# Kernel tuning notes

Hardware: AMD Instinct MI355X
Metric: run time of the kernel (lower is better)

The kernel has to match this reference:

```python
import jax, jax.numpy as jnp
import numpy as np
from jax import lax

B, K, C = 8, 65536, 128
NUM_PROPOSAL = 1024


def furthest_point_sample(xyz, n):
    """xyz: (B,K,3) -> (B,n) int32 indices, matching pointnet2 FPS."""
    b, k, _ = xyz.shape
    init_far = jnp.zeros((b,), dtype=jnp.int32)          # first picked point = index 0
    init_dist = jnp.full((b, k), 1e10, dtype=xyz.dtype)  # running min squared distance

    def step(carry, _):
        dist, far = carry
        pt = jnp.take_along_axis(xyz, far[:, None, None].astype(jnp.int32), axis=1)  # (B,1,3)
        d = jnp.sum((xyz - pt) ** 2, axis=-1)            # (B,K)
        dist = jnp.minimum(dist, d)
        far = jnp.argmax(dist, axis=-1).astype(jnp.int32)
        return (dist, far), far

    (_, _), rest = lax.scan(step, (init_dist, init_far), None, length=n - 1)  # rest: (n-1,B)
    inds = jnp.concatenate([init_far[None, :], rest], axis=0)                  # (n,B)
    return jnp.transpose(inds, (1, 0))                                         # (B,n)


def setup_inputs() -> dict:
    key = jax.random.key(0)
    k1, k2 = jax.random.split(key)
    xyz = jax.random.normal(k1, (B, K, 3), dtype=jnp.float32)
    features = jax.random.normal(k2, (B, C, K), dtype=jnp.float32)
    return {"xyz": xyz, "features": features}


def reference(xyz, features):
    sample_inds = furthest_point_sample(xyz, NUM_PROPOSAL)            # (B,n)
    # gather_operation(xyz^T, inds)^T -> (B,n,3)
    new_xyz = jnp.take_along_axis(xyz, sample_inds[:, :, None], axis=1)
    # gather_operation(features, inds) -> (B,C,n)
    new_features = jnp.take_along_axis(features, sample_inds[:, None, :], axis=2)
    return (new_xyz, new_features, sample_inds)
```

## Files before the change

### kernel.cpp

```cpp
#include <hip/hip_runtime.h>
#include <stdint.h>

#define BATCH 8
#define K 65536
#define CFEAT 128
#define NPROP 1024
#define M 16
#define T 256
#define PTS (K / M)
#define PPT (PTS / T)

#define OUT_FEAT (BATCH * NPROP * 3)
#define OUT_INDS (BATCH * NPROP * 3 + BATCH * CFEAT * NPROP)

#define SLOT_STRIDE 8
#define WS_ULLS (2 * BATCH * M * SLOT_STRIDE)

__global__ __launch_bounds__(256) void fps_init(unsigned long long* ws) {
    int i = blockIdx.x * 256 + threadIdx.x;
    if (i < WS_ULLS) ws[i] = 0ull;
}

__device__ __forceinline__ unsigned int wave_umax63(unsigned int x) {
    int v = (int)x;
    int t;
    t = __builtin_amdgcn_update_dpp(v, v, 0x111, 0xF, 0xF, false);
    v = ((unsigned)t > (unsigned)v) ? t : v;
    t = __builtin_amdgcn_update_dpp(v, v, 0x112, 0xF, 0xF, false);
    v = ((unsigned)t > (unsigned)v) ? t : v;
    t = __builtin_amdgcn_update_dpp(v, v, 0x114, 0xF, 0xF, false);
    v = ((unsigned)t > (unsigned)v) ? t : v;
    t = __builtin_amdgcn_update_dpp(v, v, 0x118, 0xF, 0xF, false);
    v = ((unsigned)t > (unsigned)v) ? t : v;
    t = __builtin_amdgcn_update_dpp(v, v, 0x142, 0xF, 0xF, false);
    v = ((unsigned)t > (unsigned)v) ? t : v;
    t = __builtin_amdgcn_update_dpp(v, v, 0x143, 0xF, 0xF, false);
    v = ((unsigned)t > (unsigned)v) ? t : v;
    return (unsigned int)v;
}

__device__ __forceinline__ unsigned int row16_umax15(unsigned int x) {
    int v = (int)x;
    int t;
    t = __builtin_amdgcn_update_dpp(v, v, 0x111, 0xF, 0xF, false);
    v = ((unsigned)t > (unsigned)v) ? t : v;
    t = __builtin_amdgcn_update_dpp(v, v, 0x112, 0xF, 0xF, false);
    v = ((unsigned)t > (unsigned)v) ? t : v;
    t = __builtin_amdgcn_update_dpp(v, v, 0x114, 0xF, 0xF, false);
    v = ((unsigned)t > (unsigned)v) ? t : v;
    t = __builtin_amdgcn_update_dpp(v, v, 0x118, 0xF, 0xF, false);
    v = ((unsigned)t > (unsigned)v) ? t : v;
    return (unsigned int)v;
}

__global__ __launch_bounds__(T) void fps_kernel(const float* __restrict__ xyz,
                                                float* __restrict__ out,
                                                unsigned long long* __restrict__ ws) {
    const int b = blockIdx.x & 7;
    const int w = blockIdx.x >> 3;
    const int tid = threadIdx.x;
    const int lane = tid & 63;
    const int wv = tid >> 6;
    const float* xb = xyz + (size_t)b * (K * 3);
    const int base = w * PTS;

    __shared__ unsigned long long s_wkey[T / 64];
    __shared__ int s_g;

    float px[PPT], py[PPT], pz[PPT], dist[PPT];
#pragma unroll
    for (int j = 0; j < PPT; ++j) {
        int l = j * T + tid;
        int g = base + l;
        px[j] = xb[3 * g];
        py[j] = xb[3 * g + 1];
        pz[j] = xb[3 * g + 2];
        dist[j] = 1e10f;
    }
    float qx = xb[0], qy = xb[1], qz = xb[2];
    if (w == 0 && tid == 0) out[OUT_INDS + b * NPROP] = 0.0f;

    for (int t = 1; t < NPROP; ++t) {
        float bestd = -1.0f;
        unsigned int bestl = 0;
#pragma unroll
        for (int j = 0; j < PPT; ++j) {
            float dx = __fsub_rn(px[j], qx);
            float dy = __fsub_rn(py[j], qy);
            float dz = __fsub_rn(pz[j], qz);
            float d = __fadd_rn(__fadd_rn(__fmul_rn(dx, dx), __fmul_rn(dy, dy)),
                                __fmul_rn(dz, dz));
            float nd = fminf(dist[j], d);
            dist[j] = nd;
            unsigned int l = (unsigned int)(j * T + tid);
            bool gt = nd > bestd;
            bestd = gt ? nd : bestd;
            bestl = gt ? l : bestl;
        }
        unsigned int du = __float_as_uint(bestd);
        unsigned int m1 = wave_umax63(du);
        unsigned int maxd = (unsigned int)__builtin_amdgcn_readlane((int)m1, 63);
        unsigned int cand = (du == maxd) ? ~bestl : 0u;
        unsigned int m2 = wave_umax63(cand);

        const int par = t & 1;
        unsigned long long* sgrp = ws + (size_t)((par * BATCH + b) * M) * SLOT_STRIDE;
        const unsigned int tt = (unsigned int)t;

        if (lane == 63) {
            unsigned int l = ~m2;
            unsigned int g = (unsigned int)base + l;
            s_wkey[wv] = ((unsigned long long)maxd << 32) |
                         ((unsigned long long)((0xFFFFu - g) & 0xFFFFu) << 16) |
                         (unsigned long long)tt;
        }
        __syncthreads();

        if (tid == 0) {
            unsigned long long kb = s_wkey[0];
#pragma unroll
            for (int i = 1; i < T / 64; ++i) kb = (s_wkey[i] > kb) ? s_wkey[i] : kb;
            __hip_atomic_store(&sgrp[(size_t)w * SLOT_STRIDE], kb,
                               __ATOMIC_RELAXED, __HIP_MEMORY_SCOPE_AGENT);
        }

        if (tid < M) {
            unsigned long long* sp = sgrp + (size_t)tid * SLOT_STRIDE;
            unsigned long long k;
            do {
                k = __hip_atomic_load(sp, __ATOMIC_RELAXED, __HIP_MEMORY_SCOPE_AGENT);
            } while ((unsigned short)k != (unsigned short)tt);
            unsigned int hi = (unsigned int)(k >> 32);
            unsigned int lo = (unsigned int)k;
            unsigned int p1 = row16_umax15(hi);
            unsigned int maxk = (unsigned int)__builtin_amdgcn_readlane((int)p1, 15);
            unsigned int c2 = (hi == maxk) ? lo : 0u;
            unsigned int p2 = row16_umax15(c2);
            unsigned int low = (unsigned int)__builtin_amdgcn_readlane((int)p2, 15);
            unsigned int g = 0xFFFFu - (low >> 16);
            if (tid == 0) {
                s_g = (int)g;
                if (w == 0) out[OUT_INDS + b * NPROP + t] = (float)g;
            }
        }
        __syncthreads();
        int g = s_g;
        qx = xb[3 * g];
        qy = xb[3 * g + 1];
        qz = xb[3 * g + 2];
    }
}

__global__ __launch_bounds__(256) void gather_kernel(const float* __restrict__ xyz,
                                                     const float* __restrict__ feat,
                                                     float* __restrict__ out) {
    int gid = blockIdx.x * 256 + threadIdx.x;
    int n = gid & (NPROP - 1);
    int b = gid >> 17;
    int c = (gid >> 10) & (CFEAT - 1);
    int ind = (int)out[OUT_INDS + (b << 10) + n];
    out[OUT_FEAT + gid] = feat[(((size_t)b * CFEAT + c) << 16) + (size_t)ind];
    if (gid < BATCH * NPROP) {
        int b2 = gid >> 10;
        int ind2 = (int)out[OUT_INDS + gid];
        const float* s = xyz + ((size_t)b2 * K + (size_t)ind2) * 3;
        float a0 = s[0], a1 = s[1], a2 = s[2];
        out[gid * 3 + 0] = a0;
        out[gid * 3 + 1] = a1;
        out[gid * 3 + 2] = a2;
    }
}

extern "C" void kernel_launch(void* const* d_in, const int* in_sizes, int n_in,
                              void* d_out, int out_size, void* d_ws, size_t ws_size,
                              hipStream_t stream) {
    const float* xyz = (const float*)d_in[0];
    const float* feat = (const float*)d_in[1];
    float* out = (float*)d_out;
    unsigned long long* ws = (unsigned long long*)d_ws;

    hipLaunchKernelGGL(fps_init, dim3(WS_ULLS / 256), dim3(256), 0, stream, ws);
    hipLaunchKernelGGL(fps_kernel, dim3(BATCH * M), dim3(T), 0, stream,
                       xyz, out, ws);
    hipLaunchKernelGGL(gather_kernel, dim3(BATCH * CFEAT * NPROP / 256), dim3(256),
                       0, stream, xyz, feat, out);
}
```

Measured before the change: 1.972 ms.

## Prefetch candidate coordinates during cross-block poll and use LDS atomic max

Each of the 16 polling lanes loads its own candidate's coordinates as soon as its slot is ready, then the winning lane's coordinates are broadcast with ds_bpermute. This takes the dependent global load of the winning point off the critical path after the final barrier. The per-wave key reduction now uses an LDS atomicMax instead of a serial loop in thread 0, and polling is double-issued with a wave-wide __all exit. In exchange, all 16 lanes issue extra global loads, polling traffic goes up, and the ping-pong s_kmax must be reset correctly.

```diff
diff --git a/kernel.cpp b/kernel.cpp
--- a/kernel.cpp
+++ b/kernel.cpp
@@ -60,12 +60,11 @@
     const int w = blockIdx.x >> 3;
     const int tid = threadIdx.x;
     const int lane = tid & 63;
-    const int wv = tid >> 6;
     const float* xb = xyz + (size_t)b * (K * 3);
     const int base = w * PTS;
 
-    __shared__ unsigned long long s_wkey[T / 64];
-    __shared__ int s_g;
+    __shared__ unsigned long long s_kmax[2];
+    __shared__ float s_qx, s_qy, s_qz;
 
     float px[PPT], py[PPT], pz[PPT], dist[PPT];
 #pragma unroll
@@ -78,7 +77,9 @@
         dist[j] = 1e10f;
     }
     float qx = xb[0], qy = xb[1], qz = xb[2];
+    if (tid == 0) { s_kmax[0] = 0ull; s_kmax[1] = 0ull; }
     if (w == 0 && tid == 0) out[OUT_INDS + b * NPROP] = 0.0f;
+    __syncthreads();
 
     for (int t = 1; t < NPROP; ++t) {
         float bestd = -1.0f;
@@ -110,26 +111,39 @@
         if (lane == 63) {
             unsigned int l = ~m2;
             unsigned int g = (unsigned int)base + l;
-            s_wkey[wv] = ((unsigned long long)maxd << 32) |
-                         ((unsigned long long)((0xFFFFu - g) & 0xFFFFu) << 16) |
-                         (unsigned long long)tt;
+            unsigned long long key = ((unsigned long long)maxd << 32) |
+                                     ((unsigned long long)((0xFFFFu - g) & 0xFFFFu) << 16) |
+                                     (unsigned long long)tt;
+            atomicMax(&s_kmax[par], key);
         }
         __syncthreads();
 
         if (tid == 0) {
-            unsigned long long kb = s_wkey[0];
-#pragma unroll
-            for (int i = 1; i < T / 64; ++i) kb = (s_wkey[i] > kb) ? s_wkey[i] : kb;
+            unsigned long long kb = s_kmax[par];
+            s_kmax[par] = 0ull;
             __hip_atomic_store(&sgrp[(size_t)w * SLOT_STRIDE], kb,
                                __ATOMIC_RELAXED, __HIP_MEMORY_SCOPE_AGENT);
         }
 
         if (tid < M) {
             unsigned long long* sp = sgrp + (size_t)tid * SLOT_STRIDE;
-            unsigned long long k;
-            do {
-                k = __hip_atomic_load(sp, __ATOMIC_RELAXED, __HIP_MEMORY_SCOPE_AGENT);
-            } while ((unsigned short)k != (unsigned short)tt);
+            unsigned long long a = __hip_atomic_load(sp, __ATOMIC_RELAXED,
+                                                     __HIP_MEMORY_SCOPE_AGENT);
+            unsigned long long bq = __hip_atomic_load(sp, __ATOMIC_RELAXED,
+                                                      __HIP_MEMORY_SCOPE_AGENT);
+            unsigned long long k = 0ull;
+            bool got = false;
+            for (;;) {
+                if (!got && (unsigned short)a == (unsigned short)tt) { k = a; got = true; }
+                if (__all(got)) break;
+                a = __hip_atomic_load(sp, __ATOMIC_RELAXED, __HIP_MEMORY_SCOPE_AGENT);
+                if (!got && (unsigned short)bq == (unsigned short)tt) { k = bq; got = true; }
+                if (__all(got)) break;
+                bq = __hip_atomic_load(sp, __ATOMIC_RELAXED, __HIP_MEMORY_SCOPE_AGENT);
+            }
+            unsigned int gl = 0xFFFFu - (unsigned int)((k >> 16) & 0xFFFFu);
+            const float* cp = xb + 3 * (size_t)gl;
+            float cxl = cp[0], cyl = cp[1], czl = cp[2];
             unsigned int hi = (unsigned int)(k >> 32);
             unsigned int lo = (unsigned int)k;
             unsigned int p1 = row16_umax15(hi);
@@ -138,16 +152,21 @@
             unsigned int p2 = row16_umax15(c2);
             unsigned int low = (unsigned int)__builtin_amdgcn_readlane((int)p2, 15);
             unsigned int g = 0xFFFFu - (low >> 16);
+            int s = (int)(g >> 12);
+            int ad = s << 2;
+            float wx = __uint_as_float((unsigned int)__builtin_amdgcn_ds_bpermute(
+                ad, (int)__float_as_uint(cxl)));
+            float wy = __uint_as_float((unsigned int)__builtin_amdgcn_ds_bpermute(
+                ad, (int)__float_as_uint(cyl)));
+            float wz = __uint_as_float((unsigned int)__builtin_amdgcn_ds_bpermute(
+                ad, (int)__float_as_uint(czl)));
             if (tid == 0) {
-                s_g = (int)g;
+                s_qx = wx; s_qy = wy; s_qz = wz;
                 if (w == 0) out[OUT_INDS + b * NPROP + t] = (float)g;
             }
         }
         __syncthreads();
-        int g = s_g;
-        qx = xb[3 * g];
-        qy = xb[3 * g + 1];
-        qz = xb[3 * g + 2];
+        qx = s_qx; qy = s_qy; qz = s_qz;
     }
 }
 
```

Result: slower. 2.082 ms (+5.6%).

## Publish winner coordinates in mirrored slots and poll via sc0 line loads

Applied to the files above, without the earlier changes.

Each workgroup now publishes its best candidate's key and its xyz coordinates into a mirror cache line. Pollers read the whole line with sc0 vector loads for a bounded number of tries, then fall back to the atomic slot. The global winner's coordinates are taken from the winning slot with ds_bpermute, which removes the dependent global load of the next query point after the barrier. This shortens the serial critical path of every FPS iteration, at the cost of extra stores and inline asm that depends on cache-coherence behaviour.

```diff
diff --git a/kernel.cpp b/kernel.cpp
--- a/kernel.cpp
+++ b/kernel.cpp
@@ -14,7 +14,11 @@
 #define OUT_INDS (BATCH * NPROP * 3 + BATCH * CFEAT * NPROP)
 
 #define SLOT_STRIDE 8
-#define WS_ULLS (2 * BATCH * M * SLOT_STRIDE)
+#define MIRROR_ULLS (2 * BATCH * M * SLOT_STRIDE)
+#define WS_ULLS (2 * MIRROR_ULLS)
+#define FAST_ITERS 24
+
+typedef unsigned int u32x4 __attribute__((ext_vector_type(4)));
 
 __global__ __launch_bounds__(256) void fps_init(unsigned long long* ws) {
     int i = blockIdx.x * 256 + threadIdx.x;
@@ -51,6 +55,16 @@
     t = __builtin_amdgcn_update_dpp(v, v, 0x118, 0xF, 0xF, false);
     v = ((unsigned)t > (unsigned)v) ? t : v;
     return (unsigned int)v;
+}
+
+__device__ __forceinline__ void load_line_sc0(const unsigned long long* p,
+                                              u32x4& a, u32x4& bq) {
+    asm volatile("global_load_dwordx4 %0, %2, off sc0\n\t"
+                 "global_load_dwordx4 %1, %2, off offset:16 sc0\n\t"
+                 "s_waitcnt vmcnt(0)"
+                 : "=&v"(a), "=&v"(bq)
+                 : "v"(p)
+                 : "memory");
 }
 
 __global__ __launch_bounds__(T) void fps_kernel(const float* __restrict__ xyz,
@@ -65,7 +79,7 @@
     const int base = w * PTS;
 
     __shared__ unsigned long long s_wkey[T / 64];
-    __shared__ int s_g;
+    __shared__ float s_qx, s_qy, s_qz;
 
     float px[PPT], py[PPT], pz[PPT], dist[PPT];
 #pragma unroll
@@ -104,7 +118,8 @@
         unsigned int m2 = wave_umax63(cand);
 
         const int par = t & 1;
-        unsigned long long* sgrp = ws + (size_t)((par * BATCH + b) * M) * SLOT_STRIDE;
+        unsigned long long* mgrp = ws + (size_t)((par * BATCH + b) * M) * SLOT_STRIDE;
+        unsigned long long* sgrp = mgrp + MIRROR_ULLS;
         const unsigned int tt = (unsigned int)t;
 
         if (lane == 63) {
@@ -116,38 +131,86 @@
         }
         __syncthreads();
 
-        if (tid == 0) {
+        if (tid == 64) {
             unsigned long long kb = s_wkey[0];
 #pragma unroll
             for (int i = 1; i < T / 64; ++i) kb = (s_wkey[i] > kb) ? s_wkey[i] : kb;
+            unsigned int gw = 0xFFFFu - (unsigned int)((kb >> 16) & 0xFFFFu);
+            volatile unsigned long long* mme =
+                (volatile unsigned long long*)(mgrp + (size_t)w * SLOT_STRIDE);
+            mme[0] = kb;
             __hip_atomic_store(&sgrp[(size_t)w * SLOT_STRIDE], kb,
                                __ATOMIC_RELAXED, __HIP_MEMORY_SCOPE_AGENT);
+            const float* cp = xb + 3 * (size_t)gw;
+            float cx = cp[0], cy = cp[1], cz = cp[2];
+            unsigned long long tagHi = ((unsigned long long)tt) << 32;
+            mme[1] = tagHi | __float_as_uint(cz);
+            mme[2] = tagHi | __float_as_uint(cx);
+            mme[3] = tagHi | __float_as_uint(cy);
         }
 
         if (tid < M) {
-            unsigned long long* sp = sgrp + (size_t)tid * SLOT_STRIDE;
-            unsigned long long k;
-            do {
-                k = __hip_atomic_load(sp, __ATOMIC_RELAXED, __HIP_MEMORY_SCOPE_AGENT);
-            } while ((unsigned short)k != (unsigned short)tt);
-            unsigned int hi = (unsigned int)(k >> 32);
-            unsigned int lo = (unsigned int)k;
+            const unsigned long long* mp = mgrp + (size_t)tid * SLOT_STRIDE;
+            unsigned long long kk = 0ull;
+            unsigned int zv = 0, zt = 0, xv = 0, xt = 0, yv = 0, yt = 0;
+            bool have = false;
+            for (int it = 0; it < FAST_ITERS && !have; ++it) {
+                u32x4 a, bq;
+                load_line_sc0(mp, a, bq);
+                if ((a.x & 0xFFFFu) == tt) {
+                    kk = ((unsigned long long)a.y << 32) | a.x;
+                    zv = a.z; zt = a.w; xv = bq.x; xt = bq.y; yv = bq.z; yt = bq.w;
+                    have = true;
+                }
+            }
+            if (!have) {
+                unsigned long long* sp = sgrp + (size_t)tid * SLOT_STRIDE;
+                unsigned long long v;
+                do {
+                    v = __hip_atomic_load(sp, __ATOMIC_RELAXED, __HIP_MEMORY_SCOPE_AGENT);
+                } while ((unsigned short)v != (unsigned short)tt);
+                kk = v;
+            }
+            unsigned int hi = (unsigned int)(kk >> 32);
+            unsigned int lo = (unsigned int)kk;
             unsigned int p1 = row16_umax15(hi);
             unsigned int maxk = (unsigned int)__builtin_amdgcn_readlane((int)p1, 15);
             unsigned int c2 = (hi == maxk) ? lo : 0u;
             unsigned int p2 = row16_umax15(c2);
             unsigned int low = (unsigned int)__builtin_amdgcn_readlane((int)p2, 15);
             unsigned int g = 0xFFFFu - (low >> 16);
+            int s = (int)(g >> 12);
+            int ad = s << 2;
+            unsigned int wzv = (unsigned int)__builtin_amdgcn_ds_bpermute(ad, (int)zv);
+            unsigned int wzt = (unsigned int)__builtin_amdgcn_ds_bpermute(ad, (int)zt);
+            unsigned int wxv = (unsigned int)__builtin_amdgcn_ds_bpermute(ad, (int)xv);
+            unsigned int wxt = (unsigned int)__builtin_amdgcn_ds_bpermute(ad, (int)xt);
+            unsigned int wyv = (unsigned int)__builtin_amdgcn_ds_bpermute(ad, (int)yv);
+            unsigned int wyt = (unsigned int)__builtin_amdgcn_ds_bpermute(ad, (int)yt);
+            float wx, wy, wz;
+            if (wzt == tt && wxt == tt && wyt == tt) {
+                wx = __uint_as_float(wxv);
+                wy = __uint_as_float(wyv);
+                wz = __uint_as_float(wzv);
+            } else {
+                u32x4 a2, b2;
+                load_line_sc0(mgrp + (size_t)s * SLOT_STRIDE, a2, b2);
+                if (a2.w == tt && b2.y == tt && b2.w == tt) {
+                    wz = __uint_as_float(a2.z);
+                    wx = __uint_as_float(b2.x);
+                    wy = __uint_as_float(b2.z);
+                } else {
+                    const float* cp = xb + 3 * (size_t)g;
+                    wx = cp[0]; wy = cp[1]; wz = cp[2];
+                }
+            }
             if (tid == 0) {
-                s_g = (int)g;
+                s_qx = wx; s_qy = wy; s_qz = wz;
                 if (w == 0) out[OUT_INDS + b * NPROP + t] = (float)g;
             }
         }
         __syncthreads();
-        int g = s_g;
-        qx = xb[3 * g];
-        qy = xb[3 * g + 1];
-        qz = xb[3 * g + 2];
+        qx = s_qx; qy = s_qy; qz = s_qz;
     }
 }
 
```

Result: slower. 5.307 ms (+169.1%).

## Add dedicated coordinator wave replacing block barriers with LDS flag spinning

Applied to the files above, without the earlier changes.

Adds a fifth wavefront per block that collects the four compute waves' keys from shared memory, publishes the block key to global workspace, polls the other blocks and writes the winner to a shared result word. Compute waves no longer call __syncthreads each iteration; they spin on the shared result word tagged with the iteration number. The aim is to remove block-wide barrier latency from the 1023-step serial loop. It relies on relaxed atomics and spin-waiting within a workgroup, and the extra wave competes with the compute waves for issue slots.

```diff
diff --git a/kernel.cpp b/kernel.cpp
--- a/kernel.cpp
+++ b/kernel.cpp
@@ -6,9 +6,10 @@
 #define CFEAT 128
 #define NPROP 1024
 #define M 16
-#define T 256
+#define T 320
+#define CTHREADS 256
 #define PTS (K / M)
-#define PPT (PTS / T)
+#define PPT (PTS / CTHREADS)
 
 #define OUT_FEAT (BATCH * NPROP * 3)
 #define OUT_INDS (BATCH * NPROP * 3 + BATCH * CFEAT * NPROP)
@@ -64,90 +65,123 @@
     const float* xb = xyz + (size_t)b * (K * 3);
     const int base = w * PTS;
 
-    __shared__ unsigned long long s_wkey[T / 64];
-    __shared__ int s_g;
+    __shared__ unsigned long long s_wkey[4];
+    __shared__ unsigned int s_res;
 
     float px[PPT], py[PPT], pz[PPT], dist[PPT];
-#pragma unroll
-    for (int j = 0; j < PPT; ++j) {
-        int l = j * T + tid;
-        int g = base + l;
-        px[j] = xb[3 * g];
-        py[j] = xb[3 * g + 1];
-        pz[j] = xb[3 * g + 2];
-        dist[j] = 1e10f;
-    }
-    float qx = xb[0], qy = xb[1], qz = xb[2];
-    if (w == 0 && tid == 0) out[OUT_INDS + b * NPROP] = 0.0f;
-
-    for (int t = 1; t < NPROP; ++t) {
-        float bestd = -1.0f;
-        unsigned int bestl = 0;
+    if (wv < 4) {
 #pragma unroll
         for (int j = 0; j < PPT; ++j) {
-            float dx = __fsub_rn(px[j], qx);
-            float dy = __fsub_rn(py[j], qy);
-            float dz = __fsub_rn(pz[j], qz);
-            float d = __fadd_rn(__fadd_rn(__fmul_rn(dx, dx), __fmul_rn(dy, dy)),
-                                __fmul_rn(dz, dz));
-            float nd = fminf(dist[j], d);
-            dist[j] = nd;
-            unsigned int l = (unsigned int)(j * T + tid);
-            bool gt = nd > bestd;
-            bestd = gt ? nd : bestd;
-            bestl = gt ? l : bestl;
+            int l = j * CTHREADS + tid;
+            int g = base + l;
+            px[j] = xb[3 * g];
+            py[j] = xb[3 * g + 1];
+            pz[j] = xb[3 * g + 2];
+            dist[j] = 1e10f;
         }
-        unsigned int du = __float_as_uint(bestd);
-        unsigned int m1 = wave_umax63(du);
-        unsigned int maxd = (unsigned int)__builtin_amdgcn_readlane((int)m1, 63);
-        unsigned int cand = (du == maxd) ? ~bestl : 0u;
-        unsigned int m2 = wave_umax63(cand);
-
-        const int par = t & 1;
-        unsigned long long* sgrp = ws + (size_t)((par * BATCH + b) * M) * SLOT_STRIDE;
-        const unsigned int tt = (unsigned int)t;
-
-        if (lane == 63) {
-            unsigned int l = ~m2;
-            unsigned int g = (unsigned int)base + l;
-            s_wkey[wv] = ((unsigned long long)maxd << 32) |
-                         ((unsigned long long)((0xFFFFu - g) & 0xFFFFu) << 16) |
-                         (unsigned long long)tt;
+    }
+    float qx = xb[0], qy = xb[1], qz = xb[2];
+    if (tid == 0) {
+        s_wkey[0] = 0ull; s_wkey[1] = 0ull; s_wkey[2] = 0ull; s_wkey[3] = 0ull;
+        s_res = 0u;
+        if (w == 0) out[OUT_INDS + b * NPROP] = 0.0f;
+    }
+    __syncthreads();
+
+    if (wv < 4) {
+        for (int t = 1; t < NPROP; ++t) {
+            float bestd = -1.0f;
+            unsigned int bestl = 0;
+#pragma unroll
+            for (int j = 0; j < PPT; ++j) {
+                float dx = __fsub_rn(px[j], qx);
+                float dy = __fsub_rn(py[j], qy);
+                float dz = __fsub_rn(pz[j], qz);
+                float d = __fadd_rn(__fadd_rn(__fmul_rn(dx, dx), __fmul_rn(dy, dy)),
+                                    __fmul_rn(dz, dz));
+                float nd = fminf(dist[j], d);
+                dist[j] = nd;
+                unsigned int l = (unsigned int)(j * CTHREADS + tid);
+                bool gt = nd > bestd;
+                bestd = gt ? nd : bestd;
+                bestl = gt ? l : bestl;
+            }
+            unsigned int du = __float_as_uint(bestd);
+            unsigned int m1 = wave_umax63(du);
+            unsigned int maxd = (unsigned int)__builtin_amdgcn_readlane((int)m1, 63);
+            unsigned int cand = (du == maxd) ? ~bestl : 0u;
+            unsigned int m2 = wave_umax63(cand);
+            if (lane == 63) {
+                unsigned int l = ~m2;
+                unsigned int g = (unsigned int)base + l;
+                unsigned long long key =
+                    ((unsigned long long)maxd << 32) |
+                    ((unsigned long long)((0xFFFFu - g) & 0xFFFFu) << 16) |
+                    (unsigned long long)(unsigned int)t;
+                __hip_atomic_store(&s_wkey[wv], key, __ATOMIC_RELAXED,
+                                   __HIP_MEMORY_SCOPE_WORKGROUP);
+            }
+            unsigned int r;
+            do {
+                r = __hip_atomic_load(&s_res, __ATOMIC_RELAXED,
+                                      __HIP_MEMORY_SCOPE_WORKGROUP);
+            } while ((r & 0xFFFFu) != (unsigned int)t);
+            unsigned int g = r >> 16;
+            qx = xb[3 * g];
+            qy = xb[3 * g + 1];
+            qz = xb[3 * g + 2];
         }
-        __syncthreads();
-
-        if (tid == 0) {
-            unsigned long long kb = s_wkey[0];
-#pragma unroll
-            for (int i = 1; i < T / 64; ++i) kb = (s_wkey[i] > kb) ? s_wkey[i] : kb;
-            __hip_atomic_store(&sgrp[(size_t)w * SLOT_STRIDE], kb,
-                               __ATOMIC_RELAXED, __HIP_MEMORY_SCOPE_AGENT);
-        }
-
-        if (tid < M) {
-            unsigned long long* sp = sgrp + (size_t)tid * SLOT_STRIDE;
-            unsigned long long k;
-            do {
-                k = __hip_atomic_load(sp, __ATOMIC_RELAXED, __HIP_MEMORY_SCOPE_AGENT);
-            } while ((unsigned short)k != (unsigned short)tt);
-            unsigned int hi = (unsigned int)(k >> 32);
-            unsigned int lo = (unsigned int)k;
-            unsigned int p1 = row16_umax15(hi);
-            unsigned int maxk = (unsigned int)__builtin_amdgcn_readlane((int)p1, 15);
-            unsigned int c2 = (hi == maxk) ? lo : 0u;
-            unsigned int p2 = row16_umax15(c2);
-            unsigned int low = (unsigned int)__builtin_amdgcn_readlane((int)p2, 15);
-            unsigned int g = 0xFFFFu - (low >> 16);
-            if (tid == 0) {
-                s_g = (int)g;
-                if (w == 0) out[OUT_INDS + b * NPROP + t] = (float)g;
+    } else {
+        for (int t = 1; t < NPROP; ++t) {
+            const int par = t & 1;
+            unsigned long long* sgrp =
+                ws + (size_t)((par * BATCH + b) * M) * SLOT_STRIDE;
+            const unsigned int tt = (unsigned int)t;
+            if (lane < M) {
+                unsigned long long kk;
+                do {
+                    kk = __hip_atomic_load(&s_wkey[lane & 3], __ATOMIC_RELAXED,
+                                           __HIP_MEMORY_SCOPE_WORKGROUP);
+                } while ((kk & 0xFFFFu) != (unsigned long long)tt);
+                unsigned int hi = (unsigned int)(kk >> 32);
+                unsigned int lo = (unsigned int)kk;
+                unsigned int p1 = row16_umax15(hi);
+                unsigned int mh = (unsigned int)__builtin_amdgcn_readlane((int)p1, 15);
+                unsigned int c2 = (hi == mh) ? lo : 0u;
+                unsigned int p2 = row16_umax15(c2);
+                unsigned int ml = (unsigned int)__builtin_amdgcn_readlane((int)p2, 15);
+                if (lane == 0) {
+                    unsigned long long kb = ((unsigned long long)mh << 32) |
+                                            (unsigned long long)ml;
+                    __hip_atomic_store(&sgrp[(size_t)w * SLOT_STRIDE], kb,
+                                       __ATOMIC_RELAXED, __HIP_MEMORY_SCOPE_AGENT);
+                }
+                unsigned int khi, klo;
+                if (lane == w) {
+                    khi = mh; klo = ml;
+                } else {
+                    unsigned long long* sp = sgrp + (size_t)lane * SLOT_STRIDE;
+                    unsigned long long v;
+                    do {
+                        v = __hip_atomic_load(sp, __ATOMIC_RELAXED,
+                                              __HIP_MEMORY_SCOPE_AGENT);
+                    } while ((unsigned short)v != (unsigned short)tt);
+                    khi = (unsigned int)(v >> 32);
+                    klo = (unsigned int)v;
+                }
+                unsigned int q1 = row16_umax15(khi);
+                unsigned int qh = (unsigned int)__builtin_amdgcn_readlane((int)q1, 15);
+                unsigned int d2 = (khi == qh) ? klo : 0u;
+                unsigned int q2 = row16_umax15(d2);
+                unsigned int ql = (unsigned int)__builtin_amdgcn_readlane((int)q2, 15);
+                unsigned int g = 0xFFFFu - (ql >> 16);
+                if (lane == 0) {
+                    __hip_atomic_store(&s_res, (g << 16) | tt, __ATOMIC_RELAXED,
+                                       __HIP_MEMORY_SCOPE_WORKGROUP);
+                    if (w == 0) out[OUT_INDS + b * NPROP + t] = (float)g;
+                }
             }
         }
-        __syncthreads();
-        int g = s_g;
-        qx = xb[3 * g];
-        qy = xb[3 * g + 1];
-        qz = xb[3 * g + 2];
     }
 }
 
```

Measured after the change: 2.021 ms. 1.02x slower.
